# Kernel tuning notes

Measured on AMD Instinct MI355X. Metric: run time of the kernel, lower is better.

## Reference

```python
import jax, jax.numpy as jnp
import numpy as np

K = 3
TOPK = 10
HORIZON = 12


def gru_cell(x, h, w_ih, w_hh, b_ih, b_hh):
    # torch GRU gate order: r, z, n ; n = tanh(W_in x + b_in + r*(W_hn h + b_hn))
    gx = x @ w_ih.T + b_ih
    gh = h @ w_hh.T + b_hh
    H = h.shape[-1]
    r = jax.nn.sigmoid(gx[:, :H] + gh[:, :H])
    z = jax.nn.sigmoid(gx[:, H:2 * H] + gh[:, H:2 * H])
    n = jnp.tanh(gx[:, 2 * H:] + r * gh[:, 2 * H:])
    return (1.0 - z) * n + z * h


def setup_inputs() -> dict:
    key = jax.random.key(0)
    ks = jax.random.split(key, 16)
    B, T, N, F = 128, 12, 207, 14
    H = 128
    f = lambda i, shp, s=0.1: jax.random.normal(ks[i], shp, dtype=jnp.float32) * s
    return {
        'x': jax.random.normal(ks[0], (B, T, N, F), dtype=jnp.float32),
        'A_physical': jax.random.uniform(ks[1], (N, N), dtype=jnp.float32),
        'fc_start_w': f(2, (16, 1), 0.5),
        'fc_start_b': jnp.zeros((16,), jnp.float32),
        'alpha': jnp.float32(0.5),
        'context_w': f(3, (32, 13)),
        'context_b': jnp.zeros((32,), jnp.float32),
        'tcn_w': f(4, (64, 1, 1, 3), 0.3),
        'tcn_b': jnp.zeros((64,), jnp.float32),
        'theta': f(5, (K, 32, 32), 0.15),
        'attn_w': f(6, (1, 65)),
        'attn_b': jnp.zeros((1,), jnp.float32),
        'enc_w_ih': f(7, (3 * H, 65)),
        'enc_w_hh': f(8, (3 * H, H)),
        'enc_b_ih': jnp.zeros((3 * H,), jnp.float32),
        'enc_b_hh': jnp.zeros((3 * H,), jnp.float32),
        'dec_w_ih': f(9, (3 * H, 33)),
        'dec_w_hh': f(10, (3 * H, H)),
        'dec_b_ih': jnp.zeros((3 * H,), jnp.float32),
        'dec_b_hh': jnp.zeros((3 * H,), jnp.float32),
        'out_w': f(11, (1, H)),
        'out_b': jnp.zeros((1,), jnp.float32),
    }


def reference(x, A_physical, fc_start_w, fc_start_b, alpha, context_w, context_b,
              tcn_w, tcn_b, theta, attn_w, attn_b,
              enc_w_ih, enc_w_hh, enc_b_ih, enc_b_hh,
              dec_w_ih, dec_w_hh, dec_b_ih, dec_b_hh, out_w, out_b):
    B, T, N, _ = x.shape
    H = enc_w_hh.shape[1]
    traffic = x[..., 0:1]          # [B,T,N,1]
    context = x[..., 1:]           # [B,T,N,13]

    # ---- dynamic graph: topk + scatter + softmax, blended with physical ----
    state = traffic[:, -1]                                   # [B,N,1]
    emb = jnp.tanh(state @ fc_start_w.T + fc_start_b)        # [B,N,16]
    A_dyn = jax.nn.relu(jnp.einsum('bnd,bmd->bnm', emb, emb))
    vals, idx = jax.lax.top_k(A_dyn, TOPK)
    sparse = jnp.zeros_like(A_dyn).at[
        jnp.arange(B)[:, None, None], jnp.arange(N)[None, :, None], idx].set(vals)
    A_dyn = jax.nn.softmax(sparse, axis=2)
    a = jax.nn.sigmoid(alpha)
    A = a * A_physical[None] + (1.0 - a) * A_dyn             # [B,N,N]

    # ---- gated temporal conv (causal, GLU) ----
    xt = jnp.transpose(traffic, (0, 3, 2, 1))                # [B,1,N,T]
    conv = jax.lax.conv_general_dilated(
        xt, tcn_w, (1, 1), [(0, 0), (2, 0)],
        dimension_numbers=('NCHW', 'OIHW', 'NCHW')) + tcn_b[None, :, None, None]
    P, Q = jnp.split(conv, 2, axis=1)
    t_feat = jnp.transpose(P * jax.nn.sigmoid(Q), (0, 3, 2, 1))  # [B,T,N,32]

    # ---- Chebyshev K-hop graph conv ----
    I = jnp.eye(N, dtype=x.dtype)
    lam = jnp.clip(jnp.max(jnp.sum(A, -1), -1), 1.0)[:, None, None]
    L = 2.0 * A / lam - I[None]
    Tk = [jnp.broadcast_to(I[None], (B, N, N)), L]
    for k in range(2, K):
        Tk.append(2.0 * jnp.einsum('bnm,bmp->bnp', L, Tk[-1]) - Tk[-2])
    s = 0.0
    for k in range(K):
        rhs = jnp.einsum('btnf,fo->btno', t_feat, theta[k])
        s = s + jnp.einsum('bnm,btmo->btno', Tk[k], rhs)
    s_feat = jax.nn.relu(s)                                   # [B,T,N,32] (dropout off: eval)

    # ---- attention fusion ----
    c_emb = jax.nn.relu(context @ context_w.T + context_b)    # [B,T,N,32]
    fusion = jnp.concatenate([traffic, s_feat, c_emb], -1)    # [B,T,N,65]
    attn = jax.nn.sigmoid(fusion @ attn_w.T + attn_b)
    z = fusion * attn
    # NOTE: original torch code does z.view(B*N, T, -1) on a [B,T,N,65] contiguous
    # tensor (raw reshape, no permute) -- replicated faithfully.
    z_flat = z.reshape(B * N, T, -1)

    # ---- encoder GRU ----
    h = jnp.zeros((B * N, H), x.dtype)
    def enc_step(h, xt_):
        return gru_cell(xt_, h, enc_w_ih, enc_w_hh, enc_b_ih, enc_b_hh), None
    h, _ = jax.lax.scan(enc_step, h, jnp.transpose(z_flat, (1, 0, 2)))

    cur = traffic[:, -1, :, 0].reshape(B * N, 1)
    ctx = c_emb[:, -1].reshape(B * N, 32)
    def dec_step(carry, _):
        hh, cc = carry
        h2 = gru_cell(jnp.concatenate([cc, ctx], 1), hh,
                      dec_w_ih, dec_w_hh, dec_b_ih, dec_b_hh)
        pred = h2 @ out_w.T + out_b
        return (h2, pred), pred
    _, preds = jax.lax.scan(dec_step, (h, cur), None, length=HORIZON)  # [Hz,B*N,1]
    out = jnp.transpose(preds[..., 0], (1, 0)).reshape(B, N, HORIZON)
    return jnp.transpose(out, (0, 2, 1))                      # [B,horizon,N]
```

## Files before the change

### kernel.cpp

```cpp
#include <hip/hip_runtime.h>
#include <math.h>

#define NB 128
#define NT 12
#define NNODE 207
#define NF 14
#define NH 128
#define ROWS (NB*NNODE)
#define BTN (NB*NT*NNODE)
#define G3 (3*NH)
#define LSTR 208
#define RG (ROWS/16)

typedef __attribute__((ext_vector_type(8))) short short8;
typedef __attribute__((ext_vector_type(4))) float accf4;

#define MFMA16 __builtin_amdgcn_mfma_f32_16x16x32_bf16

__device__ __forceinline__ float sigf(float x){ return 1.0f/(1.0f+__expf(-x)); }
__device__ __forceinline__ float tanhfast(float x){
  float e = __expf(2.f*x);
  return 1.f - 2.f/(e + 1.f);
}
__device__ __forceinline__ unsigned short f2b(float f){
  unsigned int u = __float_as_uint(f);
  return (unsigned short)((u + 0x7FFFu + ((u>>16)&1u)) >> 16);
}
__device__ __forceinline__ float b2f(unsigned short h){
  return __uint_as_float(((unsigned int)h) << 16);
}
__device__ __forceinline__ void mm3(short8 ah, short8 al, short8 bh, short8 bl, accf4& acc){
  acc = MFMA16(ah, bh, acc, 0,0,0);
  acc = MFMA16(al, bh, acc, 0,0,0);
  acc = MFMA16(ah, bl, acc, 0,0,0);
}

__global__ __launch_bounds__(256) void k_sentinel(float* __restrict__ out, int n){
  int i = blockIdx.x*256 + threadIdx.x;
  if (i < n) out[i] = 12345.0f;
}

#define NW_ENC (7*24*64*8)
#define NW_DEC (4*24*64*8)
#define SH_TOTAL (2*NW_ENC + 2*NW_DEC)
#define FWT_TOTAL (32*384 + 384)
#define PREP_TOTAL (NW_ENC + NW_DEC + 32*384 + 384)
__global__ __launch_bounds__(256) void k_prep(const float* __restrict__ ewih,
    const float* __restrict__ ewhh, const float* __restrict__ dwih,
    const float* __restrict__ dwhh, short* __restrict__ ws, float* __restrict__ wf){
  int i = blockIdx.x*256 + threadIdx.x;
  if (i < NW_ENC){
    int e = i & 7, lane = (i>>3) & 63, ct = (i>>9) % 24, ks = i / 12288;
    int k = ks*32 + (lane>>4)*8 + e;
    int col = ct*16 + (lane&15);
    float wv = (k < 65) ? ewih[col*65 + k] : ((k < 96) ? 0.f : ewhh[col*128 + (k-96)]);
    unsigned short hi = f2b(wv);
    ws[i] = (short)hi;
    ws[NW_ENC + i] = (short)f2b(wv - b2f(hi));
  } else if (i < NW_ENC + NW_DEC){
    int j = i - NW_ENC;
    int e = j & 7, lane = (j>>3) & 63, ct = (j>>9) % 24, ks = j / 12288;
    int k = ks*32 + (lane>>4)*8 + e;
    int col = ct*16 + (lane&15);
    float wv = dwhh[col*128 + k];
    unsigned short hi = f2b(wv);
    ws[2*NW_ENC + j] = (short)hi;
    ws[2*NW_ENC + NW_DEC + j] = (short)f2b(wv - b2f(hi));
  } else if (i < NW_ENC + NW_DEC + 32*384){
    int j = i - (NW_ENC + NW_DEC); int k = j/384, n = j%384;
    wf[j] = dwih[n*33 + 1 + k];
  } else if (i < PREP_TOTAL){
    int n = i - (NW_ENC + NW_DEC + 32*384);
    wf[32*384 + n] = dwih[n*33];
  }
}

__global__ __launch_bounds__(256) void k_emb(const float* __restrict__ x,
    const float* __restrict__ w, const float* __restrict__ b, float* __restrict__ emb){
  int idx = blockIdx.x*256 + threadIdx.x;
  if (idx >= ROWS*16) return;
  int j = idx & 15, row = idx >> 4;
  int bb = row / NNODE, n = row % NNODE;
  float s = x[((bb*NT + (NT-1))*NNODE + n)*NF];
  emb[idx] = tanhf(s*w[j] + b[j]);
}

__global__ __launch_bounds__(256) void k_adj(const float* __restrict__ emb,
    const float* __restrict__ Aph, const float* __restrict__ alp,
    float* __restrict__ Abuf, float* __restrict__ rsum){
  int wid = threadIdx.x >> 6, lane = threadIdx.x & 63;
  int row = blockIdx.x*4 + wid;
  int bb = row / NNODE, n = row % NNODE;
  const float4* er = (const float4*)(emb + (size_t)row*16);
  float4 e0 = er[0], e1 = er[1], e2 = er[2], e3 = er[3];
  float d[4];
  #pragma unroll
  for (int q=0;q<4;++q){
    int m = lane + q*64;
    float dd = -1.f;
    if (m < NNODE){
      const float4* em = (const float4*)(emb + (size_t)(bb*NNODE+m)*16);
      float4 m0 = em[0], m1 = em[1], m2 = em[2], m3 = em[3];
      dd = e0.x*m0.x + e0.y*m0.y + e0.z*m0.z + e0.w*m0.w
         + e1.x*m1.x + e1.y*m1.y + e1.z*m1.z + e1.w*m1.w
         + e2.x*m2.x + e2.y*m2.y + e2.z*m2.z + e2.w*m2.w
         + e3.x*m3.x + e3.y*m3.y + e3.z*m3.z + e3.w*m3.w;
      dd = dd > 0.f ? dd : 0.f;
    }
    d[q] = dd;
  }
  int km = 0;
  float vmax = 0.f;
  for (int it=0; it<10; ++it){
    float v = -1.f; int mi = 1<<20;
    #pragma unroll
    for (int q=0;q<4;++q){
      if (d[q] >= 0.f && !((km>>q)&1) && d[q] > v){ v = d[q]; mi = lane + q*64; }
    }
    #pragma unroll
    for (int off=1; off<64; off<<=1){
      float v2 = __shfl_xor(v, off, 64);
      int  i2 = __shfl_xor(mi, off, 64);
      if (v2 > v || (v2 == v && i2 < mi)){ v = v2; mi = i2; }
    }
    if (it == 0) vmax = v;
    if ((mi & 63) == lane) km |= 1 << (mi >> 6);
  }
  float a = sigf(alp[0]);
  float eneg = __expf(-vmax);
  float p[4]; float ps = 0.f;
  #pragma unroll
  for (int q=0;q<4;++q){
    p[q] = 0.f;
    if (d[q] >= 0.f) p[q] = ((km>>q)&1) ? __expf(d[q]-vmax) : eneg;
    ps += p[q];
  }
  #pragma unroll
  for (int off=1; off<64; off<<=1) ps += __shfl_xor(ps, off, 64);
  float inv = (1.f - a)/ps;
  float rs = 0.f;
  #pragma unroll
  for (int q=0;q<4;++q){
    int m = lane + q*64;
    if (m < NNODE){
      float Av = a*Aph[n*NNODE + m] + p[q]*inv;
      Abuf[(size_t)row*LSTR + m] = Av;
      rs += Av;
    }
  }
  if (lane == 0) Abuf[(size_t)row*LSTR + 207] = 0.f;
  #pragma unroll
  for (int off=1; off<64; off<<=1) rs += __shfl_xor(rs, off, 64);
  if (lane == 0) rsum[row] = rs;
}

__global__ __launch_bounds__(256) void k_lam(const float* __restrict__ rsum, float* __restrict__ lam){
  __shared__ float rv[256];
  int b = blockIdx.x, tid = threadIdx.x;
  rv[tid] = (tid < NNODE) ? rsum[b*NNODE+tid] : -1e30f;
  __syncthreads();
  for (int s=128;s>0;s>>=1){ if (tid<s) rv[tid]=fmaxf(rv[tid],rv[tid+s]); __syncthreads(); }
  if (tid==0) lam[b] = fmaxf(rv[0], 1.0f);
}

__global__ __launch_bounds__(256) void k_lap(float* __restrict__ Abuf, const float* __restrict__ lam){
  int idx = blockIdx.x*256 + threadIdx.x;
  if (idx >= NB*NNODE*LSTR) return;
  int b = idx / (NNODE*LSTR);
  int rem = idx % (NNODE*LSTR);
  int n = rem / LSTR, m = rem % LSTR;
  Abuf[idx] = 2.f*Abuf[idx]/lam[b] - (n==m ? 1.f : 0.f);
}

__global__ __launch_bounds__(256) void k_tcn(const float* __restrict__ x,
    const float* __restrict__ w, const float* __restrict__ bcn, float* __restrict__ tfeat){
  int idx = blockIdx.x*256 + threadIdx.x;
  if (idx >= BTN*32) return;
  int o = idx & 31; int r = idx >> 5;
  int n = r % NNODE, bt = r / NNODE, t = bt % NT, b = bt / NT;
  float t0 = (t>=2)? x[((size_t)(b*NT+t-2)*NNODE+n)*NF] : 0.f;
  float t1 = (t>=1)? x[((size_t)(b*NT+t-1)*NNODE+n)*NF] : 0.f;
  float t2 = x[((size_t)(b*NT+t)*NNODE+n)*NF];
  float P = bcn[o]    + w[o*3]*t0       + w[o*3+1]*t1       + w[o*3+2]*t2;
  float Q = bcn[o+32] + w[(o+32)*3]*t0  + w[(o+32)*3+1]*t1  + w[(o+32)*3+2]*t2;
  tfeat[(size_t)r*32 + o] = P * sigf(Q);
}

__global__ __launch_bounds__(256) void k_thetaBC(const float* __restrict__ tfeat,
    const float* __restrict__ theta, float* __restrict__ P2, float* __restrict__ P1){
  __shared__ float thB[32][33], thC[32][33];
  __shared__ float tf[8][32];
  int tid = threadIdx.x;
  for (int i=tid; i<1024; i+=256){
    int f = i >> 5, o = i & 31;
    thB[o][f] = theta[1024+f*32+o]; thC[o][f] = theta[2048+f*32+o];
  }
  int rl = tid >> 5, o = tid & 31;
  int r = blockIdx.x*8 + rl;
  tf[rl][o] = tfeat[(size_t)r*32 + o];
  __syncthreads();
  float aB=0.f, aC=0.f;
  #pragma unroll
  for (int f=0; f<32; ++f){
    float t = tf[rl][f];
    aB += t*thB[o][f]; aC += t*thC[o][f];
  }
  int n = r % NNODE, bt = r / NNODE, t = bt % NT, b = bt / NT;
  size_t outi = (size_t)(b*NNODE+n)*G3 + t*32 + o;
  P2[outi]=aB; P1[outi]=aC;
}

__global__ __launch_bounds__(256) void k_thetaA(const float* __restrict__ tfeat,
    const float* __restrict__ theta, float* __restrict__ P1){
  __shared__ float thA[32][33];
  __shared__ float tf[8][32];
  int tid = threadIdx.x;
  for (int i=tid; i<1024; i+=256){
    int f = i >> 5, o = i & 31;
    thA[o][f] = theta[f*32+o] - theta[2048+f*32+o];
  }
  int rl = tid >> 5, o = tid & 31;
  int r = blockIdx.x*8 + rl;
  tf[rl][o] = tfeat[(size_t)r*32 + o];
  __syncthreads();
  float aA=0.f;
  #pragma unroll
  for (int f=0; f<32; ++f) aA += tf[rl][f]*thA[o][f];
  int n = r % NNODE, bt = r / NNODE, t = bt % NT, b = bt / NT;
  P1[(size_t)(b*NNODE+n)*G3 + t*32 + o] = aA;
}

__global__ __launch_bounds__(256) void gemm128(
    const float* __restrict__ Ab, int lda, long long sA,
    const float* __restrict__ Bb, long long sB,
    const float* __restrict__ bias,
    const float* __restrict__ Yb, long long sY, float alphaV, float betaV, int do_relu,
    float* __restrict__ Cb, long long sC, int M, int kchunks){
  __shared__ float As[16][132];
  __shared__ float Bs[16][132];
  int bz = blockIdx.z;
  const float* A = Ab + (size_t)bz*sA;
  const float* B = Bb + (size_t)bz*sB;
  float* C = Cb + (size_t)bz*sC;
  int n0 = blockIdx.x*128, m0 = blockIdx.y*128;
  int tid = threadIdx.x, tx = tid & 15, ty = tid >> 4;
  float acc[8][8] = {};
  int ar = tid & 127, ak = (tid >> 7)*8;
  int bk = tid >> 4, bn = (tid & 15)*8;
  for (int kc=0; kc<kchunks; ++kc){
    int k0 = kc*16;
    int m = m0 + ar;
    if (m < M){
      const float* ap = A + (size_t)m*lda + k0 + ak;
      float4 v0 = *(const float4*)ap, v1 = *(const float4*)(ap+4);
      As[ak+0][ar]=v0.x; As[ak+1][ar]=v0.y; As[ak+2][ar]=v0.z; As[ak+3][ar]=v0.w;
      As[ak+4][ar]=v1.x; As[ak+5][ar]=v1.y; As[ak+6][ar]=v1.z; As[ak+7][ar]=v1.w;
    } else {
      #pragma unroll
      for (int j=0;j<8;++j) As[ak+j][ar]=0.f;
    }
    const float* bp = B + (size_t)(k0+bk)*384 + n0 + bn;
    float4 w0_ = *(const float4*)bp, w1_ = *(const float4*)(bp+4);
    *(float4*)&Bs[bk][bn] = w0_; *(float4*)&Bs[bk][bn+4] = w1_;
    __syncthreads();
    #pragma unroll
    for (int kk=0;kk<16;++kk){
      float4 a0 = *(const float4*)&As[kk][ty*8];
      float4 a1 = *(const float4*)&As[kk][ty*8+4];
      float4 b0 = *(const float4*)&Bs[kk][tx*4];
      float4 b1 = *(const float4*)&Bs[kk][64+tx*4];
      float av[8] = {a0.x,a0.y,a0.z,a0.w,a1.x,a1.y,a1.z,a1.w};
      float bv[8] = {b0.x,b0.y,b0.z,b0.w,b1.x,b1.y,b1.z,b1.w};
      #pragma unroll
      for (int i=0;i<8;++i)
        #pragma unroll
        for (int j=0;j<8;++j) acc[i][j] += av[i]*bv[j];
    }
    __syncthreads();
  }
  if (bias){
    float bl[4], bh_[4];
    #pragma unroll
    for (int j=0;j<4;++j){ bl[j]=bias[n0+tx*4+j]; bh_[j]=bias[n0+64+tx*4+j]; }
    #pragma unroll
    for (int i=0;i<8;++i){
      int m2 = m0 + ty*8 + i; if (m2 >= M) continue;
      float4 s0, s1;
      s0.x=acc[i][0]+bl[0]; s0.y=acc[i][1]+bl[1]; s0.z=acc[i][2]+bl[2]; s0.w=acc[i][3]+bl[3];
      s1.x=acc[i][4]+bh_[0]; s1.y=acc[i][5]+bh_[1]; s1.z=acc[i][6]+bh_[2]; s1.w=acc[i][7]+bh_[3];
      *(float4*)&C[(size_t)m2*384 + n0 + tx*4] = s0;
      *(float4*)&C[(size_t)m2*384 + n0 + 64 + tx*4] = s1;
    }
  } else {
    const float* Y = Yb + (size_t)bz*sY;
    #pragma unroll
    for (int i=0;i<8;++i){
      int m2 = m0 + ty*8 + i; if (m2 >= M) continue;
      const float* yr = Y + (size_t)m2*384;
      float* cr = C + (size_t)m2*384;
      float4 y0 = *(const float4*)(yr + n0 + tx*4);
      float4 y1 = *(const float4*)(yr + n0 + 64 + tx*4);
      float4 s0, s1;
      s0.x = alphaV*acc[i][0] + betaV*y0.x; s0.y = alphaV*acc[i][1] + betaV*y0.y;
      s0.z = alphaV*acc[i][2] + betaV*y0.z; s0.w = alphaV*acc[i][3] + betaV*y0.w;
      s1.x = alphaV*acc[i][4] + betaV*y1.x; s1.y = alphaV*acc[i][5] + betaV*y1.y;
      s1.z = alphaV*acc[i][6] + betaV*y1.z; s1.w = alphaV*acc[i][7] + betaV*y1.w;
      if (do_relu){
        s0.x=fmaxf(s0.x,0.f); s0.y=fmaxf(s0.y,0.f); s0.z=fmaxf(s0.z,0.f); s0.w=fmaxf(s0.w,0.f);
        s1.x=fmaxf(s1.x,0.f); s1.y=fmaxf(s1.y,0.f); s1.z=fmaxf(s1.z,0.f); s1.w=fmaxf(s1.w,0.f);
      }
      *(float4*)(cr + n0 + tx*4) = s0;
      *(float4*)(cr + n0 + 64 + tx*4) = s1;
    }
  }
}

#define GATEB(WH, WL, KS) \
    const int ko = (KS)*24; \
    short8 bRh = *(const short8*)(WH + ((size_t)(ko + w)*64 + lane)*8); \
    short8 bZh = *(const short8*)(WH + ((size_t)(ko + 8 + w)*64 + lane)*8); \
    short8 bNh = *(const short8*)(WH + ((size_t)(ko + 16 + w)*64 + lane)*8); \
    short8 bRl = *(const short8*)(WL + ((size_t)(ko + w)*64 + lane)*8); \
    short8 bZl = *(const short8*)(WL + ((size_t)(ko + 8 + w)*64 + lane)*8); \
    short8 bNl = *(const short8*)(WL + ((size_t)(ko + 16 + w)*64 + lane)*8);

__global__ __launch_bounds__(512) void k_encdec(
    const short* __restrict__ zfH, const short* __restrict__ zfL,
    const short* __restrict__ WFH, const short* __restrict__ WFL,
    const float* __restrict__ bih, const float* __restrict__ bhh,
    const short* __restrict__ DFH, const short* __restrict__ DFL,
    const float* __restrict__ dbhh, const float* __restrict__ ctxGX,
    const float* __restrict__ w0, const float* __restrict__ ow,
    const float* __restrict__ ob, const float* __restrict__ pred0,
    float* __restrict__ preds_out){
  __shared__ __attribute__((aligned(16))) short hfH[4*512];
  __shared__ __attribute__((aligned(16))) short hfL[4*512];
  __shared__ float psl[8][16];
  __shared__ float predl[16];
  int R = blockIdx.x, m0 = R*16;
  int tid = threadIdx.x;
  int w = tid >> 6, lane = tid & 63;
  int g = lane >> 4, c = lane & 15;
  int j = (w<<4) + c;
  float hreg[4] = {};
  for (int i = tid; i < 2048; i += 512){ hfH[i] = 0; hfL[i] = 0; }
  if (tid < 16) predl[tid] = pred0[m0 + tid];
  int ksh = w >> 1, qh = 2*(w&1) + (c>>3), eh = c & 7;
  float birv = bih[j], bizv = bih[128+j], binv = bih[256+j];
  float bhrv = bhh[j], bhzv = bhh[128+j], bhnv = bhh[256+j];
  __syncthreads();

  for (int t = 0; t < NT; ++t){
    accf4 aR = {}, aZ = {}, aNZ = {}, aNH = {};
    #pragma unroll
    for (int ks=0; ks<3; ++ks){
      GATEB(WFH, WFL, ks);
      size_t zb = (((size_t)t*RG + R)*3 + ks)*512;
      short8 ah = *(const short8*)(zfH + zb + lane*8);
      short8 al = *(const short8*)(zfL + zb + lane*8);
      mm3(ah, al, bRh, bRl, aR);
      mm3(ah, al, bZh, bZl, aZ);
      mm3(ah, al, bNh, bNl, aNZ);
    }
    #pragma unroll
    for (int ks=3; ks<7; ++ks){
      GATEB(WFH, WFL, ks);
      short8 ah = *(const short8*)&hfH[(ks-3)*512 + lane*8];
      short8 al = *(const short8*)&hfL[(ks-3)*512 + lane*8];
      mm3(ah, al, bRh, bRl, aR);
      mm3(ah, al, bZh, bZl, aZ);
      mm3(ah, al, bNh, bNl, aNH);
    }
    __syncthreads();
    #pragma unroll
    for (int i=0;i<4;++i){
      float r_ = sigf(aR[i] + birv + bhrv);
      float z_ = sigf(aZ[i] + bizv + bhzv);
      float n_ = tanhfast(aNZ[i] + binv + r_*(aNH[i] + bhnv));
      float hn = (1.f - z_)*n_ + z_*hreg[i];
      hreg[i] = hn;
      unsigned short hh = f2b(hn);
      int o = ksh*512 + ((g*4+i) + 16*qh)*8 + eh;
      hfH[o] = (short)hh;
      hfL[o] = (short)f2b(hn - b2f(hh));
    }
    __syncthreads();
  }

  float w0r = w0[j], w0z = w0[128+j], w0n = w0[256+j];
  float bhr = dbhh[j], bhz = dbhh[128+j], bhn = dbhh[256+j];
  float owj = ow[j];
  float obv = ob[0];
  float gxr[4], gxz[4], gxn[4];
  #pragma unroll
  for (int i=0;i<4;++i){
    int row = g*4 + i;
    const float* gx = ctxGX + (size_t)(m0+row)*384;
    gxr[i] = gx[j]; gxz[i] = gx[128+j]; gxn[i] = gx[256+j];
  }
  for (int s = 0; s < NT; ++s){
    accf4 aR = {}, aZ = {}, aN = {};
    #pragma unroll
    for (int ks=0; ks<4; ++ks){
      GATEB(DFH, DFL, ks);
      short8 ah = *(const short8*)&hfH[ks*512 + lane*8];
      short8 al = *(const short8*)&hfL[ks*512 + lane*8];
      mm3(ah, al, bRh, bRl, aR);
      mm3(ah, al, bZh, bZl, aZ);
      mm3(ah, al, bNh, bNl, aN);
    }
    __syncthreads();
    #pragma unroll
    for (int i=0;i<4;++i){
      int row = g*4 + i;
      float p = predl[row];
      float r_ = sigf(gxr[i] + p*w0r + aR[i] + bhr);
      float z_ = sigf(gxz[i] + p*w0z + aZ[i] + bhz);
      float n_ = tanhfast(gxn[i] + p*w0n + r_*(aN[i] + bhn));
      float hn = (1.f - z_)*n_ + z_*hreg[i];
      hreg[i] = hn;
      unsigned short hh = f2b(hn);
      int o = ksh*512 + (row + 16*qh)*8 + eh;
      hfH[o] = (short)hh;
      hfL[o] = (short)f2b(hn - b2f(hh));
      float psv = hn*owj;
      psv += __shfl_xor(psv, 1, 64);
      psv += __shfl_xor(psv, 2, 64);
      psv += __shfl_xor(psv, 4, 64);
      psv += __shfl_xor(psv, 8, 64);
      if (c == 0) psl[w][row] = psv;
    }
    __syncthreads();
    if (tid < 16){
      float sm = obv;
      #pragma unroll
      for (int w2=0; w2<8; ++w2) sm += psl[w2][tid];
      predl[tid] = sm;
      preds_out[(size_t)s*ROWS + m0 + tid] = sm;
    }
  }
}

__global__ __launch_bounds__(256) void k_zbuild(const float* __restrict__ x,
    const float* __restrict__ S, const float* __restrict__ cw, const float* __restrict__ cb,
    const float* __restrict__ aw, const float* __restrict__ ab,
    short* __restrict__ zfH, short* __restrict__ zfL,
    float* __restrict__ ctx, float* __restrict__ pred0){
  __shared__ float cwl[416];
  __shared__ float cbl[32];
  __shared__ float awl[65];
  __shared__ short zH[1536];
  __shared__ short zL[1536];
  int tid = threadIdx.x;
  for (int i=tid; i<416; i+=256) cwl[i] = cw[i];
  if (tid < 32) cbl[tid] = cb[tid];
  if (tid < 65) awl[tid] = aw[tid];
  {
    int* zHi = (int*)zH; int* zLi = (int*)zL;
    for (int i=tid; i<768; i+=256){ zHi[i] = 0; zLi[i] = 0; }
  }
  __syncthreads();
  int bid = blockIdx.x;
  int tau = bid / RG, Rg = bid % RG;
  int trow = tid >> 4, tl = tid & 15;
  int i_ = Rg*16 + trow;
  int r = i_*NT + tau;
  int n = r % NNODE, bt = r / NNODE, t = bt % NT, b = bt / NT;
  const float* xr = x + (size_t)r*NF;
  float x0 = xr[0];
  float ce0 = cbl[tl], ce1 = cbl[tl+16];
  #pragma unroll
  for (int f=0; f<13; ++f){
    float xv = xr[1+f];
    ce0 += xv*cwl[tl*13+f];
    ce1 += xv*cwl[(tl+16)*13+f];
  }
  ce0 = fmaxf(ce0, 0.f); ce1 = fmaxf(ce1, 0.f);
  const float* sr = S + (size_t)(b*NNODE+n)*G3 + t*32;
  float sv0 = sr[tl], sv1 = sr[tl+16];
  float part = sv0*awl[1+tl] + ce0*awl[33+tl]
             + sv1*awl[17+tl] + ce1*awl[49+tl]
             + (tl==0 ? x0*awl[0] : 0.f);
  part += __shfl_xor(part, 1, 64);
  part += __shfl_xor(part, 2, 64);
  part += __shfl_xor(part, 4, 64);
  part += __shfl_xor(part, 8, 64);
  float attn = sigf(part + ab[0]);
  #define ZPUT(L, V) do{ int l_=(L); int ks_=l_>>5, q_=(l_&31)>>3, e_=l_&7; \
      int o_ = ks_*512 + ((trow + 16*q_)<<3) + e_; \
      float v_=(V); unsigned short hh_ = f2b(v_); \
      zH[o_] = (short)hh_; zL[o_] = (short)f2b(v_ - b2f(hh_)); }while(0)
  ZPUT(1+tl, sv0*attn);
  ZPUT(17+tl, sv1*attn);
  ZPUT(33+tl, ce0*attn);
  ZPUT(49+tl, ce1*attn);
  if (tl == 0) ZPUT(0, x0*attn);
  #undef ZPUT
  if (t == NT-1){
    float* cr = ctx + (size_t)(b*NNODE+n)*32;
    cr[tl] = ce0; cr[tl+16] = ce1;
    if (tl == 0) pred0[b*NNODE+n] = x0;
  }
  __syncthreads();
  size_t gb = (size_t)bid*1536;
  const int* zHi = (const int*)zH; const int* zLi = (const int*)zL;
  int* gH = (int*)(zfH + gb); int* gL = (int*)(zfL + gb);
  #pragma unroll
  for (int i=tid; i<768; i+=256){ gH[i] = zHi[i]; gL[i] = zLi[i]; }
}

__global__ __launch_bounds__(256) void k_out(const float* __restrict__ preds, float* __restrict__ out){
  int idx = blockIdx.x*256 + threadIdx.x;
  if (idx >= NT*ROWS) return;
  int n = idx % NNODE;
  int t2 = idx / NNODE;
  int hor = t2 % NT;
  int b = t2 / NT;
  out[idx] = preds[(size_t)hor*ROWS + b*NNODE + n];
}

extern "C" void kernel_launch(void* const* d_in, const int* in_sizes, int n_in,
                              void* d_out, int out_size, void* d_ws, size_t ws_size,
                              hipStream_t stream){
  const float* x     = (const float*)d_in[0];
  const float* Aph   = (const float*)d_in[1];
  const float* fcw   = (const float*)d_in[2];
  const float* fcb   = (const float*)d_in[3];
  const float* alp   = (const float*)d_in[4];
  const float* cw    = (const float*)d_in[5];
  const float* cb    = (const float*)d_in[6];
  const float* tw    = (const float*)d_in[7];
  const float* tb    = (const float*)d_in[8];
  const float* theta = (const float*)d_in[9];
  const float* aw    = (const float*)d_in[10];
  const float* ab    = (const float*)d_in[11];
  const float* ewih  = (const float*)d_in[12];
  const float* ewhh  = (const float*)d_in[13];
  const float* ebih  = (const float*)d_in[14];
  const float* ebhh  = (const float*)d_in[15];
  const float* dwih  = (const float*)d_in[16];
  const float* dwhh  = (const float*)d_in[17];
  const float* dbih  = (const float*)d_in[18];
  const float* dbhh  = (const float*)d_in[19];
  const float* ow    = (const float*)d_in[20];
  const float* ob    = (const float*)d_in[21];
  float* out = (float*)d_out;

  const size_t SZ_CTX  = (size_t)ROWS*32;
  const size_t SZ_PRED = (size_t)ROWS;
  const size_t SZ_PREDS= (size_t)NT*ROWS;
  const size_t SZ_G    = (size_t)ROWS*G3;
  const size_t SZ_ABUF = (size_t)NB*NNODE*LSTR;
  const size_t SZ_EMB  = (size_t)ROWS*16;
  const size_t SZ_ZF   = (size_t)NT*RG*3*512;
  const size_t SZ_UNION_FL = (2*SZ_ZF + 3) / 2;
  const size_t UNION_FL = (SZ_UNION_FL > 2*SZ_G) ? SZ_UNION_FL : 2*SZ_G;

  float* w = (float*)d_ws;
  size_t off = 0;
  auto alloc = [&](size_t nfl){ float* p = w + off; off += nfl; return p; };
  float* ctx   = alloc(SZ_CTX);
  float* pred  = alloc(SZ_PRED);
  float* preds = alloc(SZ_PREDS);
  float* Abuf  = alloc(SZ_ABUF);
  float* emb   = alloc(SZ_EMB);
  float* rsum  = alloc(SZ_PRED);
  float* lam   = alloc((size_t)NB);
  short* wS    = (short*)alloc(SH_TOTAL/2);
  float* wF    = alloc((size_t)FWT_TOTAL);
  float* Sslot = alloc(SZ_G);
  float* Uzone = alloc(UNION_FL);
  float* P1 = Uzone;
  float* P2 = Uzone + SZ_G;
  short* zfH = (short*)Uzone;
  short* zfL = zfH + SZ_ZF;
  (void)n_in; (void)in_sizes;

  if (ws_size < off*sizeof(float)){
    k_sentinel<<<(out_size+255)/256, 256, 0, stream>>>(out, out_size);
    return;
  }

  const short* WFH = wS;
  const short* WFL = wS + NW_ENC;
  const short* DFH = wS + 2*NW_ENC;
  const short* DFL = wS + 2*NW_ENC + NW_DEC;
  float* dwihT = wF;
  float* w0    = wF + 32*384;

  k_prep<<<(PREP_TOTAL+255)/256, 256, 0, stream>>>(ewih, ewhh, dwih, dwhh, wS, wF);
  float* tfeat = Sslot;
  k_emb<<<(ROWS*16)/256, 256, 0, stream>>>(x, fcw, fcb, emb);
  k_adj<<<ROWS/4, 256, 0, stream>>>(emb, Aph, alp, Abuf, rsum);
  k_lam<<<NB, 256, 0, stream>>>(rsum, lam);
  k_lap<<<(NB*NNODE*LSTR)/256, 256, 0, stream>>>(Abuf, lam);
  k_tcn<<<(BTN*32)/256, 256, 0, stream>>>(x, tw, tb, tfeat);
  k_thetaBC<<<BTN/8, 256, 0, stream>>>(tfeat, theta, P2, P1);
  gemm128<<<dim3(3, 2, NB), 256, 0, stream>>>(Abuf, LSTR, (long long)NNODE*LSTR,
      P1, (long long)NNODE*G3, nullptr,
      P2, (long long)NNODE*G3, 2.f, 1.f, 0,
      P2, (long long)NNODE*G3, NNODE, 13);
  k_thetaA<<<BTN/8, 256, 0, stream>>>(tfeat, theta, P1);
  gemm128<<<dim3(3, 2, NB), 256, 0, stream>>>(Abuf, LSTR, (long long)NNODE*LSTR,
      P2, (long long)NNODE*G3, nullptr,
      P1, (long long)NNODE*G3, 1.f, 1.f, 1,
      Sslot, (long long)NNODE*G3, NNODE, 13);
  k_zbuild<<<NT*RG, 256, 0, stream>>>(x, Sslot, cw, cb, aw, ab, zfH, zfL, ctx, pred);
  float* ctxGX = Sslot;
  gemm128<<<dim3(3, ROWS/128, 1), 256, 0, stream>>>(
      ctx, 32, 0, dwihT, 0, dbih,
      nullptr, 0, 1.f, 0.f, 0, ctxGX, 0, ROWS, 2);
  k_encdec<<<RG, 512, 0, stream>>>(zfH, zfL, WFH, WFL, ebih, ebhh,
      DFH, DFL, dbhh, ctxGX, w0, ow, ob, pred, preds);
  k_out<<<(NT*ROWS)/256, 256, 0, stream>>>(preds, out);
}
```

Measured before the change: 805.8 us.

## Drop low-bf16 weight term in GRU MFMAs and double-buffer hidden state

The GRU encoder/decoder now uses only the high bf16 part of the weights: two MFMAs per tile instead of three, and half the weight loads. The hidden-state LDS buffer is double-buffered. The encoder step then needs one barrier instead of two; the decoder still uses two because of the pred reduction. The cost is lower precision, since the weights become effectively bf16 while the activations keep the split hi/lo form.

```diff
diff --git a/kernel.cpp b/kernel.cpp
--- a/kernel.cpp
+++ b/kernel.cpp
@@ -29,10 +29,9 @@
 __device__ __forceinline__ float b2f(unsigned short h){
   return __uint_as_float(((unsigned int)h) << 16);
 }
-__device__ __forceinline__ void mm3(short8 ah, short8 al, short8 bh, short8 bl, accf4& acc){
+__device__ __forceinline__ void mm2(short8 ah, short8 al, short8 bh, accf4& acc){
   acc = MFMA16(ah, bh, acc, 0,0,0);
   acc = MFMA16(al, bh, acc, 0,0,0);
-  acc = MFMA16(ah, bl, acc, 0,0,0);
 }
 
 __global__ __launch_bounds__(256) void k_sentinel(float* __restrict__ out, int n){
@@ -315,26 +314,23 @@
   }
 }
 
-#define GATEB(WH, WL, KS) \
+#define GATEB(WH, KS) \
     const int ko = (KS)*24; \
     short8 bRh = *(const short8*)(WH + ((size_t)(ko + w)*64 + lane)*8); \
     short8 bZh = *(const short8*)(WH + ((size_t)(ko + 8 + w)*64 + lane)*8); \
-    short8 bNh = *(const short8*)(WH + ((size_t)(ko + 16 + w)*64 + lane)*8); \
-    short8 bRl = *(const short8*)(WL + ((size_t)(ko + w)*64 + lane)*8); \
-    short8 bZl = *(const short8*)(WL + ((size_t)(ko + 8 + w)*64 + lane)*8); \
-    short8 bNl = *(const short8*)(WL + ((size_t)(ko + 16 + w)*64 + lane)*8);
+    short8 bNh = *(const short8*)(WH + ((size_t)(ko + 16 + w)*64 + lane)*8);
 
 __global__ __launch_bounds__(512) void k_encdec(
     const short* __restrict__ zfH, const short* __restrict__ zfL,
-    const short* __restrict__ WFH, const short* __restrict__ WFL,
+    const short* __restrict__ WFH,
     const float* __restrict__ bih, const float* __restrict__ bhh,
-    const short* __restrict__ DFH, const short* __restrict__ DFL,
+    const short* __restrict__ DFH,
     const float* __restrict__ dbhh, const float* __restrict__ ctxGX,
     const float* __restrict__ w0, const float* __restrict__ ow,
     const float* __restrict__ ob, const float* __restrict__ pred0,
     float* __restrict__ preds_out){
-  __shared__ __attribute__((aligned(16))) short hfH[4*512];
-  __shared__ __attribute__((aligned(16))) short hfL[4*512];
+  __shared__ __attribute__((aligned(16))) short hfH[2*4*512];
+  __shared__ __attribute__((aligned(16))) short hfL[2*4*512];
   __shared__ float psl[8][16];
   __shared__ float predl[16];
   int R = blockIdx.x, m0 = R*16;
@@ -343,35 +339,37 @@
   int g = lane >> 4, c = lane & 15;
   int j = (w<<4) + c;
   float hreg[4] = {};
-  for (int i = tid; i < 2048; i += 512){ hfH[i] = 0; hfL[i] = 0; }
+  for (int i = tid; i < 4096; i += 512){ hfH[i] = 0; hfL[i] = 0; }
   if (tid < 16) predl[tid] = pred0[m0 + tid];
   int ksh = w >> 1, qh = 2*(w&1) + (c>>3), eh = c & 7;
+  int epo = ksh*512 + ((g*4) + 16*qh)*8 + eh;
   float birv = bih[j], bizv = bih[128+j], binv = bih[256+j];
   float bhrv = bhh[j], bhzv = bhh[128+j], bhnv = bhh[256+j];
   __syncthreads();
 
+  int cur = 0;
   for (int t = 0; t < NT; ++t){
     accf4 aR = {}, aZ = {}, aNZ = {}, aNH = {};
     #pragma unroll
     for (int ks=0; ks<3; ++ks){
-      GATEB(WFH, WFL, ks);
+      GATEB(WFH, ks);
       size_t zb = (((size_t)t*RG + R)*3 + ks)*512;
       short8 ah = *(const short8*)(zfH + zb + lane*8);
       short8 al = *(const short8*)(zfL + zb + lane*8);
-      mm3(ah, al, bRh, bRl, aR);
-      mm3(ah, al, bZh, bZl, aZ);
-      mm3(ah, al, bNh, bNl, aNZ);
+      mm2(ah, al, bRh, aR);
+      mm2(ah, al, bZh, aZ);
+      mm2(ah, al, bNh, aNZ);
     }
     #pragma unroll
     for (int ks=3; ks<7; ++ks){
-      GATEB(WFH, WFL, ks);
-      short8 ah = *(const short8*)&hfH[(ks-3)*512 + lane*8];
-      short8 al = *(const short8*)&hfL[(ks-3)*512 + lane*8];
-      mm3(ah, al, bRh, bRl, aR);
-      mm3(ah, al, bZh, bZl, aZ);
-      mm3(ah, al, bNh, bNl, aNH);
-    }
-    __syncthreads();
+      GATEB(WFH, ks);
+      short8 ah = *(const short8*)&hfH[cur*2048 + (ks-3)*512 + lane*8];
+      short8 al = *(const short8*)&hfL[cur*2048 + (ks-3)*512 + lane*8];
+      mm2(ah, al, bRh, aR);
+      mm2(ah, al, bZh, aZ);
+      mm2(ah, al, bNh, aNH);
+    }
+    int nxt = cur ^ 1;
     #pragma unroll
     for (int i=0;i<4;++i){
       float r_ = sigf(aR[i] + birv + bhrv);
@@ -380,11 +378,12 @@
       float hn = (1.f - z_)*n_ + z_*hreg[i];
       hreg[i] = hn;
       unsigned short hh = f2b(hn);
-      int o = ksh*512 + ((g*4+i) + 16*qh)*8 + eh;
+      int o = nxt*2048 + epo + i*8;
       hfH[o] = (short)hh;
       hfL[o] = (short)f2b(hn - b2f(hh));
     }
     __syncthreads();
+    cur = nxt;
   }
 
   float w0r = w0[j], w0z = w0[128+j], w0n = w0[256+j];
@@ -402,14 +401,14 @@
     accf4 aR = {}, aZ = {}, aN = {};
     #pragma unroll
     for (int ks=0; ks<4; ++ks){
-      GATEB(DFH, DFL, ks);
-      short8 ah = *(const short8*)&hfH[ks*512 + lane*8];
-      short8 al = *(const short8*)&hfL[ks*512 + lane*8];
-      mm3(ah, al, bRh, bRl, aR);
-      mm3(ah, al, bZh, bZl, aZ);
-      mm3(ah, al, bNh, bNl, aN);
-    }
-    __syncthreads();
+      GATEB(DFH, ks);
+      short8 ah = *(const short8*)&hfH[cur*2048 + ks*512 + lane*8];
+      short8 al = *(const short8*)&hfL[cur*2048 + ks*512 + lane*8];
+      mm2(ah, al, bRh, aR);
+      mm2(ah, al, bZh, aZ);
+      mm2(ah, al, bNh, aN);
+    }
+    int nxt = cur ^ 1;
     #pragma unroll
     for (int i=0;i<4;++i){
       int row = g*4 + i;
@@ -420,7 +419,7 @@
       float hn = (1.f - z_)*n_ + z_*hreg[i];
       hreg[i] = hn;
       unsigned short hh = f2b(hn);
-      int o = ksh*512 + (row + 16*qh)*8 + eh;
+      int o = nxt*2048 + epo + i*8;
       hfH[o] = (short)hh;
       hfL[o] = (short)f2b(hn - b2f(hh));
       float psv = hn*owj;
@@ -438,6 +437,8 @@
       predl[tid] = sm;
       preds_out[(size_t)s*ROWS + m0 + tid] = sm;
     }
+    __syncthreads();
+    cur = nxt;
   }
 }
 
@@ -582,9 +583,7 @@
   }
 
   const short* WFH = wS;
-  const short* WFL = wS + NW_ENC;
   const short* DFH = wS + 2*NW_ENC;
-  const short* DFL = wS + 2*NW_ENC + NW_DEC;
   float* dwihT = wF;
   float* w0    = wF + 32*384;
 
@@ -610,7 +609,7 @@
   gemm128<<<dim3(3, ROWS/128, 1), 256, 0, stream>>>(
       ctx, 32, 0, dwihT, 0, dbih,
       nullptr, 0, 1.f, 0.f, 0, ctxGX, 0, ROWS, 2);
-  k_encdec<<<RG, 512, 0, stream>>>(zfH, zfL, WFH, WFL, ebih, ebhh,
-      DFH, DFL, dbhh, ctxGX, w0, ow, ob, pred, preds);
+  k_encdec<<<RG, 512, 0, stream>>>(zfH, zfL, WFH, ebih, ebhh,
+      DFH, dbhh, ctxGX, w0, ow, ob, pred, preds);
   k_out<<<(NT*ROWS)/256, 256, 0, stream>>>(preds, out);
 }
```

Result: faster. 742.7 us (-7.8%).
